# Kernel tuning notes

Hardware: AMD Instinct MI355X
Metric: run time of the kernel (lower is better)

The kernel has to match this reference:

```python
import jax, jax.numpy as jnp
import numpy as np

N_NODES = 100000
N_EDGES = 1600000
D = 64
N_GRAPHS = 64


def setup_inputs() -> dict:
    key = jax.random.key(0)
    ks = jax.random.split(key, 8)
    x = jax.random.normal(ks[0], (N_NODES, D), dtype=jnp.float32)
    edge_index = jax.random.randint(ks[1], (2, N_EDGES), 0, N_NODES)
    batch = jnp.sort(jax.random.randint(ks[2], (N_NODES,), 0, N_GRAPHS))
    edge_weight = jax.random.uniform(ks[3], (N_EDGES,), dtype=jnp.float32)
    s = 1.0 / np.sqrt(D)
    W1 = jax.random.normal(ks[4], (D, D), dtype=jnp.float32) * s
    b1 = jnp.zeros((D,), dtype=jnp.float32)
    W2 = jax.random.normal(ks[5], (D, D), dtype=jnp.float32) * s
    b2 = jnp.zeros((D,), dtype=jnp.float32)
    return {"x": x, "edge_index": edge_index, "batch": batch,
            "edge_weight": edge_weight, "W1": W1, "b1": b1, "W2": W2, "b2": b2}


def reference(x, edge_index, batch, edge_weight, W1, b1, W2, b2):
    # --- GCN normalization with self-loops (PyG gcn_norm, fill_value=1) ---
    loop = jnp.arange(N_NODES)
    src = jnp.concatenate([edge_index[0], loop])
    dst = jnp.concatenate([edge_index[1], loop])
    ew = jnp.concatenate([edge_weight, jnp.ones((N_NODES,), x.dtype)])
    deg = jax.ops.segment_sum(ew, dst, num_segments=N_NODES)
    dinv = jnp.where(deg > 0, jax.lax.rsqrt(deg), 0.0)
    norm = dinv[src] * ew * dinv[dst]  # [E+N]

    def gcn_relu(h, W, b):
        h = h @ W                                   # [N, D]
        msg = h[src] * norm[:, None]                # gather + weight messages
        agg = jax.ops.segment_sum(msg, dst, num_segments=N_NODES)
        return jax.nn.relu(agg + b)

    h = gcn_relu(x, W1, b1)
    h = gcn_relu(h, W2, b2)

    # --- global mean pool over graphs ---
    sums = jax.ops.segment_sum(h, batch, num_segments=N_GRAPHS)
    counts = jax.ops.segment_sum(jnp.ones((N_NODES, 1), h.dtype), batch,
                                 num_segments=N_GRAPHS)
    return sums / jnp.maximum(counts, 1.0)
```

## Files before the change

### kernel.cpp

```cpp
#include <hip/hip_runtime.h>

#define N_NODES 100000
#define N_EDGES 1600000
#define D 64
#define N_GRAPHS 64
#define NBLK ((N_NODES + 255) / 256)
#define WTS 68

__global__ void k_init(float* __restrict__ deg, int* __restrict__ cnt,
                       float* __restrict__ out) {
    int i = blockIdx.x * blockDim.x + threadIdx.x;
    if (i < N_NODES) { deg[i] = 1.0f; cnt[i] = 0; }
    if (i < N_GRAPHS * D) out[i] = 0.0f;
}

__global__ void k_count_deg(const int* __restrict__ dst, const float* __restrict__ ew,
                            float* __restrict__ deg, int* __restrict__ cnt) {
    int e = blockIdx.x * blockDim.x + threadIdx.x;
    if (e < N_EDGES) {
        int d = dst[e];
        atomicAdd(&deg[d], ew[e]);
        atomicAdd(&cnt[d], 1);
    }
}

__global__ void k_dinv(float* __restrict__ deg) {
    int i = blockIdx.x * blockDim.x + threadIdx.x;
    if (i < N_NODES) {
        float d = deg[i];
        deg[i] = d > 0.f ? rsqrtf(d) : 0.f;
    }
}

__global__ void k_scan1(const int* __restrict__ cnt, int* __restrict__ partial,
                        int* __restrict__ bsums) {
    int t = threadIdx.x, b = blockIdx.x, i = b * 256 + t;
    int v = (i < N_NODES) ? cnt[i] : 0;
    int incl = v;
    int lane = t & 63;
#pragma unroll
    for (int off = 1; off < 64; off <<= 1) {
        int u = __shfl_up(incl, off);
        if (lane >= off) incl += u;
    }
    __shared__ int wsum[4];
    int w = t >> 6;
    if (lane == 63) wsum[w] = incl;
    __syncthreads();
    int add = 0;
    for (int k = 0; k < w; ++k) add += wsum[k];
    incl += add;
    if (i < N_NODES) partial[i] = incl;
    if (t == 255) bsums[b] = incl;
}

__global__ void k_scan2(int* __restrict__ bsums) {
    __shared__ int s[512];
    int t = threadIdx.x;
    s[t] = (t < NBLK) ? bsums[t] : 0;
    __syncthreads();
    for (int off = 1; off < 512; off <<= 1) {
        int u = (t >= off) ? s[t - off] : 0;
        __syncthreads();
        s[t] += u;
        __syncthreads();
    }
    if (t < NBLK) bsums[t] = (t == 0) ? 0 : s[t - 1];
}

__global__ void k_scan3(const int* __restrict__ partial, const int* __restrict__ cnt,
                        const int* __restrict__ bsums, int* __restrict__ rowptr,
                        int* __restrict__ cursor) {
    int i = blockIdx.x * 256 + threadIdx.x;
    if (i < N_NODES) {
        int excl = partial[i] - cnt[i] + bsums[blockIdx.x];
        rowptr[i] = excl;
        cursor[i] = excl;
    }
}

__global__ void k_scatter(const int* __restrict__ src, const int* __restrict__ dst,
                          const float* __restrict__ ew, const float* __restrict__ dinv,
                          int* __restrict__ cursor, float2* __restrict__ csr) {
    int e = blockIdx.x * blockDim.x + threadIdx.x;
    if (e < N_EDGES) {
        int s = src[e];
        int d = dst[e];
        float nrm = dinv[s] * ew[e] * dinv[d];
        int pos = atomicAdd(&cursor[d], 1);
        csr[pos] = make_float2(__int_as_float(s), nrm);
    }
}


#define CIDX(jj) (st + ((jj) < dgm1 ? ((jj) > 0 ? (jj) : 0) : (dgm1 > 0 ? dgm1 : 0)))

template <int LAYER>
__global__ __launch_bounds__(1024) void k_layer(
        const float* __restrict__ in, const float* __restrict__ W,
        const float* __restrict__ bias, const float* __restrict__ dinv,
        const int* __restrict__ rowptr, const int* __restrict__ cnt,
        const float2* __restrict__ csr, const int* __restrict__ batch,
        float* __restrict__ outp) {
    __shared__ float WTs[D * WTS];
    __shared__ float aw[16][D];
    __shared__ float bs[D];

    {
        int t = threadIdx.x;
#pragma unroll
        for (int i = 0; i < 4; ++i) {
            int idx = t + i * 1024;
            int k = idx >> 6, c = idx & 63;
            WTs[c * WTS + k] = W[idx];
        }
        if (t < D) bs[t] = bias[t];
    }
    __syncthreads();

    const int lane = threadIdx.x & 63;
    const int wid  = threadIdx.x >> 6;
    float* awm = aw[wid];
    const float bl = bs[lane];

    int gw = (blockIdx.x * blockDim.x + threadIdx.x) >> 6;
    const int tw = (gridDim.x * blockDim.x) >> 6;

    for (int row = gw; row < N_NODES; row += tw) {
        const int st = __builtin_amdgcn_readfirstlane(rowptr[row]);
        const int dg = __builtin_amdgcn_readfirstlane(cnt[row]);
        const int dgm1 = dg - 1;
        float di = dinv[row];
        float acc = in[row * D + lane] * (di * di);

        const int passes = (dg + 7) >> 3;

        float2 e0 = csr[CIDX(0)];
        float2 e1 = csr[CIDX(1)];
        float2 e2 = csr[CIDX(2)];
        float2 e3 = csr[CIDX(3)];
        float2 e4 = csr[CIDX(4)];
        float2 e5 = csr[CIDX(5)];
        float2 e6 = csr[CIDX(6)];
        float2 e7 = csr[CIDX(7)];

        for (int p = 0; p < passes; ++p) {
            const int j = p * 8;
            const int jn = j + 8;
            float2 f0 = csr[CIDX(jn + 0)];
            float2 f1 = csr[CIDX(jn + 1)];
            float2 f2 = csr[CIDX(jn + 2)];
            float2 f3 = csr[CIDX(jn + 3)];
            float2 f4 = csr[CIDX(jn + 4)];
            float2 f5 = csr[CIDX(jn + 5)];
            float2 f6 = csr[CIDX(jn + 6)];
            float2 f7 = csr[CIDX(jn + 7)];

            float w0 = (j + 0 < dg) ? e0.y : 0.f;
            float w1 = (j + 1 < dg) ? e1.y : 0.f;
            float w2 = (j + 2 < dg) ? e2.y : 0.f;
            float w3 = (j + 3 < dg) ? e3.y : 0.f;
            float w4 = (j + 4 < dg) ? e4.y : 0.f;
            float w5 = (j + 5 < dg) ? e5.y : 0.f;
            float w6 = (j + 6 < dg) ? e6.y : 0.f;
            float w7 = (j + 7 < dg) ? e7.y : 0.f;
            int s0 = __builtin_amdgcn_readfirstlane(__float_as_int(e0.x));
            int s1 = __builtin_amdgcn_readfirstlane(__float_as_int(e1.x));
            int s2 = __builtin_amdgcn_readfirstlane(__float_as_int(e2.x));
            int s3 = __builtin_amdgcn_readfirstlane(__float_as_int(e3.x));
            int s4 = __builtin_amdgcn_readfirstlane(__float_as_int(e4.x));
            int s5 = __builtin_amdgcn_readfirstlane(__float_as_int(e5.x));
            int s6 = __builtin_amdgcn_readfirstlane(__float_as_int(e6.x));
            int s7 = __builtin_amdgcn_readfirstlane(__float_as_int(e7.x));
            float v0 = in[s0 * D + lane];
            float v1 = in[s1 * D + lane];
            float v2 = in[s2 * D + lane];
            float v3 = in[s3 * D + lane];
            float v4 = in[s4 * D + lane];
            float v5 = in[s5 * D + lane];
            float v6 = in[s6 * D + lane];
            float v7 = in[s7 * D + lane];
            acc = fmaf(v0, w0, acc);
            acc = fmaf(v1, w1, acc);
            acc = fmaf(v2, w2, acc);
            acc = fmaf(v3, w3, acc);
            acc = fmaf(v4, w4, acc);
            acc = fmaf(v5, w5, acc);
            acc = fmaf(v6, w6, acc);
            acc = fmaf(v7, w7, acc);

            e0 = f0; e1 = f1; e2 = f2; e3 = f3;
            e4 = f4; e5 = f5; e6 = f6; e7 = f7;
        }

        awm[lane] = acc;
        float r0 = 0.f, r1 = 0.f, r2 = 0.f, r3 = 0.f;
#pragma unroll
        for (int t = 0; t < 16; ++t) {
            float4 a = *(const float4*)&awm[t * 4];
            float4 w = *(const float4*)&WTs[lane * WTS + t * 4];
            r0 = fmaf(a.x, w.x, r0);
            r1 = fmaf(a.y, w.y, r1);
            r2 = fmaf(a.z, w.z, r2);
            r3 = fmaf(a.w, w.w, r3);
        }
        float r = fmaxf((r0 + r1) + (r2 + r3) + bl, 0.f);

        if (LAYER == 1) {
            outp[row * D + lane] = r;
        } else {
            atomicAdd(&outp[batch[row] * D + lane], r);
        }
    }
}

__global__ void k_finalize(float* __restrict__ out, const int* __restrict__ batch) {
    int g = blockIdx.x;
    int lane = threadIdx.x;
    int lo = 0, hi = N_NODES;
    while (lo < hi) { int m = (lo + hi) >> 1; if (batch[m] < g) lo = m + 1; else hi = m; }
    int start = lo;
    hi = N_NODES;
    while (lo < hi) { int m = (lo + hi) >> 1; if (batch[m] < g + 1) lo = m + 1; else hi = m; }
    float c = (float)(lo - start);
    out[g * D + lane] /= fmaxf(c, 1.0f);
}

extern "C" void kernel_launch(void* const* d_in, const int* in_sizes, int n_in,
                              void* d_out, int out_size, void* d_ws, size_t ws_size,
                              hipStream_t stream) {
    const float* x     = (const float*)d_in[0];
    const int*   ei    = (const int*)d_in[1];
    const int*   src   = ei;
    const int*   dst   = ei + N_EDGES;
    const int*   batch = (const int*)d_in[2];
    const float* ew    = (const float*)d_in[3];
    const float* W1    = (const float*)d_in[4];
    const float* b1    = (const float*)d_in[5];
    const float* W2    = (const float*)d_in[6];
    const float* b2    = (const float*)d_in[7];
    float* out = (float*)d_out;

    char* ws = (char*)d_ws;
    float*  bufA   = (float*)(ws);
    float2* csr    = (float2*)(ws + 25600000);
    float*  deg    = (float*)(ws + 38400000);
    int*    cnt    = (int*)(ws + 38800000);
    int*    rowptr = (int*)(ws + 39200000);
    int*    cursor = (int*)(ws + 39600000);
    int*    bsums  = (int*)(ws + 40000000);

    k_init<<<NBLK, 256, 0, stream>>>(deg, cnt, out);
    k_count_deg<<<(N_EDGES + 255) / 256, 256, 0, stream>>>(dst, ew, deg, cnt);
    k_dinv<<<NBLK, 256, 0, stream>>>(deg);
    k_scan1<<<NBLK, 256, 0, stream>>>(cnt, rowptr, bsums);
    k_scan2<<<1, 512, 0, stream>>>(bsums);
    k_scan3<<<NBLK, 256, 0, stream>>>(rowptr, cnt, bsums, rowptr, cursor);
    k_scatter<<<(N_EDGES + 255) / 256, 256, 0, stream>>>(src, dst, ew, deg, cursor, csr);

    k_layer<1><<<512, 1024, 0, stream>>>(x, W1, b1, deg, rowptr, cnt, csr, batch, bufA);
    k_layer<2><<<512, 1024, 0, stream>>>(bufA, W2, b2, deg, rowptr, cnt, csr, batch, out);
    k_finalize<<<N_GRAPHS, D, 0, stream>>>(out, batch);
}
```

Measured before the change: 473.4 us.

## Split aggregation into feature-sliced gather kernels separate from per-row GEMM

Node features are stored in eight 8-column slices so each aggregation block gathers from a 3.2 MB table. The aim is to keep the random gathers cache-resident instead of streaming full 256-byte rows from HBM. Aggregation and the dense 64x64 transform become separate kernels, and the first GEMM writes its output directly in the sliced layout. This costs an extra slicing pass, eight re-reads of the CSR, and an intermediate aggregate buffer. The dinv computation is also folded into the first scan kernel, and a fallback path remains for smaller workspaces.

```diff
diff --git a/kernel.cpp b/kernel.cpp
--- a/kernel.cpp
+++ b/kernel.cpp
@@ -6,6 +6,7 @@
 #define N_GRAPHS 64
 #define NBLK ((N_NODES + 255) / 256)
 #define WTS 68
+#define NS8 (N_NODES * 8)
 
 __global__ void k_init(float* __restrict__ deg, int* __restrict__ cnt,
                        float* __restrict__ out) {
@@ -24,17 +25,13 @@
     }
 }
 
-__global__ void k_dinv(float* __restrict__ deg) {
-    int i = blockIdx.x * blockDim.x + threadIdx.x;
+__global__ void k_scan1(const int* __restrict__ cnt, int* __restrict__ partial,
+                        int* __restrict__ bsums, float* __restrict__ deg) {
+    int t = threadIdx.x, b = blockIdx.x, i = b * 256 + t;
     if (i < N_NODES) {
         float d = deg[i];
         deg[i] = d > 0.f ? rsqrtf(d) : 0.f;
     }
-}
-
-__global__ void k_scan1(const int* __restrict__ cnt, int* __restrict__ partial,
-                        int* __restrict__ bsums) {
-    int t = threadIdx.x, b = blockIdx.x, i = b * 256 + t;
     int v = (i < N_NODES) ? cnt[i] : 0;
     int incl = v;
     int lane = t & 63;
@@ -92,11 +89,133 @@
     }
 }
 
-
-#define CIDX(jj) (st + ((jj) < dgm1 ? ((jj) > 0 ? (jj) : 0) : (dgm1 > 0 ? dgm1 : 0)))
+__global__ void k_slice(const float* __restrict__ x, float* __restrict__ xs) {
+    int idx = blockIdx.x * blockDim.x + threadIdx.x;
+    const int total = N_NODES * 64;
+    const int stride = gridDim.x * blockDim.x;
+    for (; idx < total; idx += stride) {
+        int node = idx >> 6, c = idx & 63;
+        xs[(c >> 3) * NS8 + node * 8 + (c & 7)] = x[idx];
+    }
+}
+
+__global__ __launch_bounds__(256) void k_agg(
+        const float* __restrict__ tab_base,
+        const long long* __restrict__ csr64,
+        const float* __restrict__ dinv,
+        const int* __restrict__ rowptr, const int* __restrict__ cnt,
+        float* __restrict__ agg) {
+    const int s    = blockIdx.x & 7;
+    const int qb   = blockIdx.x >> 3;
+    const int bps  = gridDim.x >> 3;
+    const float* __restrict__ tab = tab_base + (size_t)s * NS8;
+    const int lane = threadIdx.x & 63;
+    const int wid  = threadIdx.x >> 6;
+    const int slot = lane >> 3;
+    const int f    = lane & 7;
+    const int wv   = qb * 4 + wid;
+    const int tws  = bps * 4;
+
+    for (int row = wv; row < N_NODES; row += tws) {
+        const int st = rowptr[row];
+        const int dg = cnt[row];
+        const float di = dinv[row];
+        float acc = (slot == 0) ? tab[row * 8 + f] * (di * di) : 0.f;
+        const int dgm1 = dg - 1;
+        for (int j = 0; j < dg; j += 32) {
+            int e0 = j + slot, e1 = j + 8 + slot, e2 = j + 16 + slot, e3 = j + 24 + slot;
+            long long c0 = __builtin_nontemporal_load(&csr64[st + (e0 < dgm1 ? e0 : dgm1)]);
+            long long c1 = __builtin_nontemporal_load(&csr64[st + (e1 < dgm1 ? e1 : dgm1)]);
+            long long c2 = __builtin_nontemporal_load(&csr64[st + (e2 < dgm1 ? e2 : dgm1)]);
+            long long c3 = __builtin_nontemporal_load(&csr64[st + (e3 < dgm1 ? e3 : dgm1)]);
+            int   i0 = (int)(c0 & 0xffffffffLL);
+            int   i1 = (int)(c1 & 0xffffffffLL);
+            int   i2 = (int)(c2 & 0xffffffffLL);
+            int   i3 = (int)(c3 & 0xffffffffLL);
+            float w0 = (e0 < dg) ? __int_as_float((int)(c0 >> 32)) : 0.f;
+            float w1 = (e1 < dg) ? __int_as_float((int)(c1 >> 32)) : 0.f;
+            float w2 = (e2 < dg) ? __int_as_float((int)(c2 >> 32)) : 0.f;
+            float w3 = (e3 < dg) ? __int_as_float((int)(c3 >> 32)) : 0.f;
+            float v0 = tab[i0 * 8 + f];
+            float v1 = tab[i1 * 8 + f];
+            float v2 = tab[i2 * 8 + f];
+            float v3 = tab[i3 * 8 + f];
+            acc = fmaf(v0, w0, acc);
+            acc = fmaf(v1, w1, acc);
+            acc = fmaf(v2, w2, acc);
+            acc = fmaf(v3, w3, acc);
+        }
+        acc += __shfl_xor(acc, 8);
+        acc += __shfl_xor(acc, 16);
+        acc += __shfl_xor(acc, 32);
+        if (lane < 8)
+            __builtin_nontemporal_store(acc, &agg[(size_t)row * D + s * 8 + lane]);
+    }
+}
+
+template <int MODE>
+__global__ __launch_bounds__(256) void k_gemm(
+        const float* __restrict__ inrows, const float* __restrict__ W,
+        const float* __restrict__ bias, const int* __restrict__ batch,
+        float* __restrict__ outp) {
+    __shared__ float WTs[D * WTS];
+    __shared__ float aw[4][D];
+    __shared__ float bs[D];
+    {
+        int t = threadIdx.x;
+#pragma unroll
+        for (int i = 0; i < 16; ++i) {
+            int idx = t + i * 256;
+            int k = idx >> 6, c = idx & 63;
+            WTs[c * WTS + k] = W[idx];
+        }
+        if (t < D) bs[t] = bias[t];
+    }
+    __syncthreads();
+
+    const int lane = threadIdx.x & 63;
+    const int wid  = threadIdx.x >> 6;
+    float* awm = aw[wid];
+    const float bl = bs[lane];
+
+    int gw = (blockIdx.x * blockDim.x + threadIdx.x) >> 6;
+    const int tw = (gridDim.x * blockDim.x) >> 6;
+
+    for (int row = gw; row < N_NODES; row += tw) {
+        awm[lane] = inrows[(size_t)row * D + lane];
+        float r0 = 0.f, r1 = 0.f, r2 = 0.f, r3 = 0.f;
+#pragma unroll
+        for (int t = 0; t < 16; ++t) {
+            float4 a = *(const float4*)&awm[t * 4];
+            float4 w = *(const float4*)&WTs[lane * WTS + t * 4];
+            r0 = fmaf(a.x, w.x, r0);
+            r1 = fmaf(a.y, w.y, r1);
+            r2 = fmaf(a.z, w.z, r2);
+            r3 = fmaf(a.w, w.w, r3);
+        }
+        float r = fmaxf((r0 + r1) + (r2 + r3) + bl, 0.f);
+        if (MODE == 0) {
+            outp[(lane >> 3) * NS8 + row * 8 + (lane & 7)] = r;
+        } else {
+            atomicAdd(&outp[batch[row] * D + lane], r);
+        }
+    }
+}
+
+__global__ void k_finalize(float* __restrict__ out, const int* __restrict__ batch) {
+    int g = blockIdx.x;
+    int lane = threadIdx.x;
+    int lo = 0, hi = N_NODES;
+    while (lo < hi) { int m = (lo + hi) >> 1; if (batch[m] < g) lo = m + 1; else hi = m; }
+    int start = lo;
+    hi = N_NODES;
+    while (lo < hi) { int m = (lo + hi) >> 1; if (batch[m] < g + 1) lo = m + 1; else hi = m; }
+    float c = (float)(lo - start);
+    out[g * D + lane] /= fmaxf(c, 1.0f);
+}
 
 template <int LAYER>
-__global__ __launch_bounds__(1024) void k_layer(
+__global__ __launch_bounds__(1024) void k_layer_fb(
         const float* __restrict__ in, const float* __restrict__ W,
         const float* __restrict__ bias, const float* __restrict__ dinv,
         const int* __restrict__ rowptr, const int* __restrict__ cnt,
@@ -105,7 +224,6 @@
     __shared__ float WTs[D * WTS];
     __shared__ float aw[16][D];
     __shared__ float bs[D];
-
     {
         int t = threadIdx.x;
 #pragma unroll
@@ -117,45 +235,29 @@
         if (t < D) bs[t] = bias[t];
     }
     __syncthreads();
-
     const int lane = threadIdx.x & 63;
     const int wid  = threadIdx.x >> 6;
     float* awm = aw[wid];
     const float bl = bs[lane];
-
     int gw = (blockIdx.x * blockDim.x + threadIdx.x) >> 6;
     const int tw = (gridDim.x * blockDim.x) >> 6;
-
     for (int row = gw; row < N_NODES; row += tw) {
         const int st = __builtin_amdgcn_readfirstlane(rowptr[row]);
         const int dg = __builtin_amdgcn_readfirstlane(cnt[row]);
         const int dgm1 = dg - 1;
         float di = dinv[row];
         float acc = in[row * D + lane] * (di * di);
-
         const int passes = (dg + 7) >> 3;
-
-        float2 e0 = csr[CIDX(0)];
-        float2 e1 = csr[CIDX(1)];
-        float2 e2 = csr[CIDX(2)];
-        float2 e3 = csr[CIDX(3)];
-        float2 e4 = csr[CIDX(4)];
-        float2 e5 = csr[CIDX(5)];
-        float2 e6 = csr[CIDX(6)];
-        float2 e7 = csr[CIDX(7)];
-
         for (int p = 0; p < passes; ++p) {
             const int j = p * 8;
-            const int jn = j + 8;
-            float2 f0 = csr[CIDX(jn + 0)];
-            float2 f1 = csr[CIDX(jn + 1)];
-            float2 f2 = csr[CIDX(jn + 2)];
-            float2 f3 = csr[CIDX(jn + 3)];
-            float2 f4 = csr[CIDX(jn + 4)];
-            float2 f5 = csr[CIDX(jn + 5)];
-            float2 f6 = csr[CIDX(jn + 6)];
-            float2 f7 = csr[CIDX(jn + 7)];
-
+            float2 e0 = csr[st + (j + 0 < dgm1 ? j + 0 : dgm1)];
+            float2 e1 = csr[st + (j + 1 < dgm1 ? j + 1 : dgm1)];
+            float2 e2 = csr[st + (j + 2 < dgm1 ? j + 2 : dgm1)];
+            float2 e3 = csr[st + (j + 3 < dgm1 ? j + 3 : dgm1)];
+            float2 e4 = csr[st + (j + 4 < dgm1 ? j + 4 : dgm1)];
+            float2 e5 = csr[st + (j + 5 < dgm1 ? j + 5 : dgm1)];
+            float2 e6 = csr[st + (j + 6 < dgm1 ? j + 6 : dgm1)];
+            float2 e7 = csr[st + (j + 7 < dgm1 ? j + 7 : dgm1)];
             float w0 = (j + 0 < dg) ? e0.y : 0.f;
             float w1 = (j + 1 < dg) ? e1.y : 0.f;
             float w2 = (j + 2 < dg) ? e2.y : 0.f;
@@ -180,19 +282,11 @@
             float v5 = in[s5 * D + lane];
             float v6 = in[s6 * D + lane];
             float v7 = in[s7 * D + lane];
-            acc = fmaf(v0, w0, acc);
-            acc = fmaf(v1, w1, acc);
-            acc = fmaf(v2, w2, acc);
-            acc = fmaf(v3, w3, acc);
-            acc = fmaf(v4, w4, acc);
-            acc = fmaf(v5, w5, acc);
-            acc = fmaf(v6, w6, acc);
-            acc = fmaf(v7, w7, acc);
-
-            e0 = f0; e1 = f1; e2 = f2; e3 = f3;
-            e4 = f4; e5 = f5; e6 = f6; e7 = f7;
-        }
-
+            acc = fmaf(v0, w0, acc); acc = fmaf(v1, w1, acc);
+            acc = fmaf(v2, w2, acc); acc = fmaf(v3, w3, acc);
+            acc = fmaf(v4, w4, acc); acc = fmaf(v5, w5, acc);
+            acc = fmaf(v6, w6, acc); acc = fmaf(v7, w7, acc);
+        }
         awm[lane] = acc;
         float r0 = 0.f, r1 = 0.f, r2 = 0.f, r3 = 0.f;
 #pragma unroll
@@ -205,25 +299,9 @@
             r3 = fmaf(a.w, w.w, r3);
         }
         float r = fmaxf((r0 + r1) + (r2 + r3) + bl, 0.f);
-
-        if (LAYER == 1) {
-            outp[row * D + lane] = r;
-        } else {
-            atomicAdd(&outp[batch[row] * D + lane], r);
-        }
-    }
-}
-
-__global__ void k_finalize(float* __restrict__ out, const int* __restrict__ batch) {
-    int g = blockIdx.x;
-    int lane = threadIdx.x;
-    int lo = 0, hi = N_NODES;
-    while (lo < hi) { int m = (lo + hi) >> 1; if (batch[m] < g) lo = m + 1; else hi = m; }
-    int start = lo;
-    hi = N_NODES;
-    while (lo < hi) { int m = (lo + hi) >> 1; if (batch[m] < g + 1) lo = m + 1; else hi = m; }
-    float c = (float)(lo - start);
-    out[g * D + lane] /= fmaxf(c, 1.0f);
+        if (LAYER == 1) outp[row * D + lane] = r;
+        else atomicAdd(&outp[batch[row] * D + lane], r);
+    }
 }
 
 extern "C" void kernel_launch(void* const* d_in, const int* in_sizes, int n_in,
@@ -240,25 +318,49 @@
     const float* W2    = (const float*)d_in[6];
     const float* b2    = (const float*)d_in[7];
     float* out = (float*)d_out;
-
     char* ws = (char*)d_ws;
-    float*  bufA   = (float*)(ws);
-    float2* csr    = (float2*)(ws + 25600000);
-    float*  deg    = (float*)(ws + 38400000);
-    int*    cnt    = (int*)(ws + 38800000);
-    int*    rowptr = (int*)(ws + 39200000);
-    int*    cursor = (int*)(ws + 39600000);
-    int*    bsums  = (int*)(ws + 40000000);
-
-    k_init<<<NBLK, 256, 0, stream>>>(deg, cnt, out);
-    k_count_deg<<<(N_EDGES + 255) / 256, 256, 0, stream>>>(dst, ew, deg, cnt);
-    k_dinv<<<NBLK, 256, 0, stream>>>(deg);
-    k_scan1<<<NBLK, 256, 0, stream>>>(cnt, rowptr, bsums);
-    k_scan2<<<1, 512, 0, stream>>>(bsums);
-    k_scan3<<<NBLK, 256, 0, stream>>>(rowptr, cnt, bsums, rowptr, cursor);
-    k_scatter<<<(N_EDGES + 255) / 256, 256, 0, stream>>>(src, dst, ew, deg, cursor, csr);
-
-    k_layer<1><<<512, 1024, 0, stream>>>(x, W1, b1, deg, rowptr, cnt, csr, batch, bufA);
-    k_layer<2><<<512, 1024, 0, stream>>>(bufA, W2, b2, deg, rowptr, cnt, csr, batch, out);
-    k_finalize<<<N_GRAPHS, D, 0, stream>>>(out, batch);
-}
+
+    if (ws_size >= 65700000) {
+        float*  xs     = (float*)(ws);
+        float*  agg    = (float*)(ws + 25600000);
+        float2* csr    = (float2*)(ws + 51200000);
+        float*  deg    = (float*)(ws + 64000000);
+        int*    cnt    = (int*)(ws + 64400000);
+        int*    rowptr = (int*)(ws + 64800000);
+        int*    cursor = (int*)(ws + 65200000);
+        int*    bsums  = (int*)(ws + 65600000);
+        const long long* csr64 = (const long long*)csr;
+
+        k_init<<<NBLK, 256, 0, stream>>>(deg, cnt, out);
+        k_count_deg<<<(N_EDGES + 255) / 256, 256, 0, stream>>>(dst, ew, deg, cnt);
+        k_scan1<<<NBLK, 256, 0, stream>>>(cnt, rowptr, bsums, deg);
+        k_scan2<<<1, 512, 0, stream>>>(bsums);
+        k_scan3<<<NBLK, 256, 0, stream>>>(rowptr, cnt, bsums, rowptr, cursor);
+        k_scatter<<<(N_EDGES + 255) / 256, 256, 0, stream>>>(src, dst, ew, deg, cursor, csr);
+
+        k_slice<<<4096, 256, 0, stream>>>(x, xs);
+        k_agg<<<4096, 256, 0, stream>>>(xs, csr64, deg, rowptr, cnt, agg);
+        k_gemm<0><<<2048, 256, 0, stream>>>(agg, W1, b1, batch, xs);
+        k_agg<<<4096, 256, 0, stream>>>(xs, csr64, deg, rowptr, cnt, agg);
+        k_gemm<1><<<2048, 256, 0, stream>>>(agg, W2, b2, batch, out);
+        k_finalize<<<N_GRAPHS, D, 0, stream>>>(out, batch);
+    } else {
+        float*  bufA   = (float*)(ws);
+        float2* csr    = (float2*)(ws + 25600000);
+        float*  deg    = (float*)(ws + 38400000);
+        int*    cnt    = (int*)(ws + 38800000);
+        int*    rowptr = (int*)(ws + 39200000);
+        int*    cursor = (int*)(ws + 39600000);
+        int*    bsums  = (int*)(ws + 40000000);
+
+        k_init<<<NBLK, 256, 0, stream>>>(deg, cnt, out);
+        k_count_deg<<<(N_EDGES + 255) / 256, 256, 0, stream>>>(dst, ew, deg, cnt);
+        k_scan1<<<NBLK, 256, 0, stream>>>(cnt, rowptr, bsums, deg);
+        k_scan2<<<1, 512, 0, stream>>>(bsums);
+        k_scan3<<<NBLK, 256, 0, stream>>>(rowptr, cnt, bsums, rowptr, cursor);
+        k_scatter<<<(N_EDGES + 255) / 256, 256, 0, stream>>>(src, dst, ew, deg, cursor, csr);
+        k_layer_fb<1><<<512, 1024, 0, stream>>>(x, W1, b1, deg, rowptr, cnt, csr, batch, bufA);
+        k_layer_fb<2><<<512, 1024, 0, stream>>>(bufA, W2, b2, deg, rowptr, cnt, csr, batch, out);
+        k_finalize<<<N_GRAPHS, D, 0, stream>>>(out, batch);
+    }
+}
```

New measurement: 798.4 us. 1.69x slower.
